# Kernel optimization log

Hardware: AMD Instinct MI355X
Metric: run time of the kernel (lower is better)

Reference implementation:

```python
import jax, jax.numpy as jnp
import numpy as np

DIM = 1024
HIDDEN = 4096
NUM_EXPERTS = 8
TOP_K = 2


def setup_inputs() -> dict:
    key = jax.random.key(0)
    ks = jax.random.split(key, 7)
    x = jax.random.normal(ks[0], (4, 2048, DIM), dtype=jnp.float32)
    # router Linear(dim, num_experts)
    Wr = jax.random.normal(ks[1], (DIM, NUM_EXPERTS), dtype=jnp.float32) / np.sqrt(DIM)
    br = jnp.zeros((NUM_EXPERTS,), dtype=jnp.float32)
    # stacked expert weights: Linear(dim, hidden) -> GELU -> Linear(hidden, dim)
    W1 = jax.random.normal(ks[2], (NUM_EXPERTS, DIM, HIDDEN), dtype=jnp.float32) / np.sqrt(DIM)
    b1 = jnp.zeros((NUM_EXPERTS, HIDDEN), dtype=jnp.float32)
    W2 = jax.random.normal(ks[3], (NUM_EXPERTS, HIDDEN, DIM), dtype=jnp.float32) / np.sqrt(HIDDEN)
    b2 = jnp.zeros((NUM_EXPERTS, DIM), dtype=jnp.float32)
    return {"x": x, "Wr": Wr, "br": br, "W1": W1, "b1": b1, "W2": W2, "b2": b2}


def reference(x, Wr, br, W1, b1, W2, b2):
    # router: g_x = W_e x ; p = softmax(g_x)
    logits = jnp.einsum('bsd,de->bse', x, Wr) + br            # [B,S,E]
    probs = jax.nn.softmax(logits, axis=-1)
    topk_probs, topk_idx = jax.lax.top_k(probs, TOP_K)        # [B,S,K]
    # dense compute-all-experts (faithful to torch.stack over experts)
    h = jnp.einsum('bsd,edh->bseh', x, W1) + b1               # [B,S,E,H]
    h = jax.nn.gelu(h, approximate=False)                      # torch nn.GELU default = exact erf
    expert_out = jnp.einsum('bseh,ehd->bsed', h, W2) + b2     # [B,S,E,D]
    # gather top-k expert outputs and mix
    selected = jnp.take_along_axis(expert_out, topk_idx[..., None], axis=2)  # [B,S,K,D]
    mixed = jnp.sum(topk_probs[..., None] * selected, axis=2)                # [B,S,D]
    return mixed, logits, probs, topk_idx, topk_probs
```

## Files before the change

### kernel.cpp

```cpp
#include <hip/hip_runtime.h>
#include <hip/hip_bf16.h>
#include <math.h>
#include <stdint.h>

#define DIMD 1024
#define HIDDEN 4096
#define NE 8
#define TOPK_ 2
#define T_TOKENS 8192
#define NROWS (T_TOKENS * TOPK_)
#define BM 128
#define BN 128
#define BK 64
#define MAXTILES (NROWS / BM + NE)
#define TGS 8
#define SPLITK 2

typedef __bf16 bf16_t;
typedef __bf16 bf16x8 __attribute__((ext_vector_type(8)));
typedef float f32x4 __attribute__((ext_vector_type(4)));

__device__ __forceinline__ void glds16(const void* g, void* l) {
    __builtin_amdgcn_global_load_lds(
        (const __attribute__((address_space(1))) unsigned int*)g,
        (__attribute__((address_space(3))) unsigned int*)l, 16, 0, 0);
}

__device__ __forceinline__ bf16x8 ldfrag(const char* lds_, int row, int kelem) {
    int byte = row * 128 + ((kelem * 2) ^ ((row & 7) << 4));
    return *reinterpret_cast<const bf16x8*>(lds_ + byte);
}

__device__ __forceinline__ int xcd_contig(int bid, int nwg) {
    int xcd = bid & 7;
    int lid = bid >> 3;
    int q = nwg >> 3, r = nwg & 7;
    int base = (xcd < r) ? xcd * (q + 1) : r * (q + 1) + (xcd - r) * q;
    return base + lid;
}

#define STAGE8(kb) do { \
    char* dA_ = lds + wid * 1024; \
    char* dB_ = lds + 16384 + wid * 1024; \
    glds16(ga0 + (kb), dA_);         glds16(gb0 + (kb), dB_); \
    glds16(ga1 + (kb), dA_ + 4096);  glds16(gb1 + (kb), dB_ + 4096); \
    glds16(ga2 + (kb), dA_ + 8192);  glds16(gb2 + (kb), dB_ + 8192); \
    glds16(ga3 + (kb), dA_ + 12288); glds16(gb3 + (kb), dB_ + 12288); \
} while (0)

#define COMPUTE64() do { \
    const char* Ab_ = lds; \
    const char* Bb_ = lds + 16384; \
    int rr_ = lane & 15, kk_ = (lane >> 4) * 8; \
    bf16x8 a_[4], b_[4]; \
    _Pragma("unroll") for (int m_ = 0; m_ < 4; ++m_) a_[m_] = ldfrag(Ab_, wr + m_ * 16 + rr_, kk_); \
    _Pragma("unroll") for (int n_ = 0; n_ < 4; ++n_) b_[n_] = ldfrag(Bb_, wc + n_ * 16 + rr_, kk_); \
    _Pragma("unroll") for (int m_ = 0; m_ < 4; ++m_) \
    _Pragma("unroll") for (int n_ = 0; n_ < 4; ++n_) \
        acc[m_][n_] = __builtin_amdgcn_mfma_f32_16x16x32_bf16(a_[m_], b_[n_], acc[m_][n_], 0, 0, 0); \
    _Pragma("unroll") for (int m_ = 0; m_ < 4; ++m_) a_[m_] = ldfrag(Ab_, wr + m_ * 16 + rr_, 32 + kk_); \
    _Pragma("unroll") for (int n_ = 0; n_ < 4; ++n_) b_[n_] = ldfrag(Bb_, wc + n_ * 16 + rr_, 32 + kk_); \
    _Pragma("unroll") for (int m_ = 0; m_ < 4; ++m_) \
    _Pragma("unroll") for (int n_ = 0; n_ < 4; ++n_) \
        acc[m_][n_] = __builtin_amdgcn_mfma_f32_16x16x32_bf16(a_[m_], b_[n_], acc[m_][n_], 0, 0, 0); \
} while (0)

#define GEMM_LOOP(nsteps) do { \
    for (int t_ = 0; t_ < (nsteps); ++t_) { \
        STAGE8(t_ * 128); \
        __syncthreads(); \
        COMPUTE64(); \
        __syncthreads(); \
    } \
} while (0)

__global__ __launch_bounds__(256) void router_kernel(
    const float* __restrict__ x, const float* __restrict__ Wr, const float* __restrict__ br,
    float* __restrict__ logits, float* __restrict__ probs,
    float* __restrict__ tidx, float* __restrict__ tprob,
    int* __restrict__ cnt, bf16_t* __restrict__ Xb)
{
    int wave = threadIdx.x >> 6;
    int lane = threadIdx.x & 63;
    int t = blockIdx.x * 4 + wave;
    if (t >= T_TOKENS) return;
    const float* xr = x + (size_t)t * DIMD;
    double acc[NE];
#pragma unroll
    for (int e = 0; e < NE; ++e) acc[e] = 0.0;
    for (int i = 0; i < DIMD / 64; ++i) {
        int d = i * 64 + lane;
        double xv = (double)xr[d];
        float4 w0 = *reinterpret_cast<const float4*>(Wr + d * NE);
        float4 w1 = *reinterpret_cast<const float4*>(Wr + d * NE + 4);
        acc[0] += xv * (double)w0.x; acc[1] += xv * (double)w0.y;
        acc[2] += xv * (double)w0.z; acc[3] += xv * (double)w0.w;
        acc[4] += xv * (double)w1.x; acc[5] += xv * (double)w1.y;
        acc[6] += xv * (double)w1.z; acc[7] += xv * (double)w1.w;
    }
#pragma unroll
    for (int s = 32; s >= 1; s >>= 1) {
#pragma unroll
        for (int e = 0; e < NE; ++e) acc[e] += __shfl_xor(acc[e], s, 64);
    }
    if (lane == 0) {
        double lg[NE], mx = -1e300;
#pragma unroll
        for (int e = 0; e < NE; ++e) { lg[e] = acc[e] + (double)br[e]; mx = fmax(mx, lg[e]); }
        int i0 = 0; double l0 = -1e300;
#pragma unroll
        for (int e = 0; e < NE; ++e) { if (lg[e] > l0) { l0 = lg[e]; i0 = e; } }
        int i1 = -1; double l1 = -1e300;
#pragma unroll
        for (int e = 0; e < NE; ++e) { if (e == i0) continue; if (lg[e] > l1) { l1 = lg[e]; i1 = e; } }
        float pe[NE], s = 0.f;
#pragma unroll
        for (int e = 0; e < NE; ++e) { pe[e] = __expf((float)(lg[e] - mx)); s += pe[e]; }
        float inv = 1.f / s;
#pragma unroll
        for (int e = 0; e < NE; ++e) {
            pe[e] *= inv;
            logits[t * NE + e] = (float)lg[e];
            probs[t * NE + e] = pe[e];
        }
        tidx[t * 2 + 0] = (float)i0; tidx[t * 2 + 1] = (float)i1;
        tprob[t * 2 + 0] = pe[i0];   tprob[t * 2 + 1] = pe[i1];
        atomicAdd(&cnt[i0], 1); atomicAdd(&cnt[i1], 1);
    }
#pragma unroll
    for (int j = 0; j < 2; ++j) {
        int i = (j * 64 + lane) * 8;
        float4 a = *reinterpret_cast<const float4*>(xr + i);
        float4 b = *reinterpret_cast<const float4*>(xr + i + 4);
        bf16x8 o;
        o[0] = (bf16_t)a.x; o[1] = (bf16_t)a.y; o[2] = (bf16_t)a.z; o[3] = (bf16_t)a.w;
        o[4] = (bf16_t)b.x; o[5] = (bf16_t)b.y; o[6] = (bf16_t)b.z; o[7] = (bf16_t)b.w;
        *reinterpret_cast<bf16x8*>(Xb + (size_t)t * DIMD + i) = o;
    }
}

__global__ __launch_bounds__(256) void transpose_kernel(
    const float* __restrict__ in, bf16_t* __restrict__ out, int K, int N)
{
    __shared__ float tile[64][33];
    int e = blockIdx.z;
    int k0 = blockIdx.x * 64;
    int n0 = blockIdx.y * 32;
    const float* ip = in + (size_t)e * K * N;
    bf16_t* op = out + (size_t)e * N * K;
    int t = threadIdx.x;
    int r = t >> 2;
    int c = (t & 3) * 8;
    float4 v0 = *reinterpret_cast<const float4*>(ip + (size_t)(k0 + r) * N + n0 + c);
    float4 v1 = *reinterpret_cast<const float4*>(ip + (size_t)(k0 + r) * N + n0 + c + 4);
    tile[r][c] = v0.x; tile[r][c + 1] = v0.y; tile[r][c + 2] = v0.z; tile[r][c + 3] = v0.w;
    tile[r][c + 4] = v1.x; tile[r][c + 5] = v1.y; tile[r][c + 6] = v1.z; tile[r][c + 7] = v1.w;
    __syncthreads();
    int nn = t >> 3;
    int kk = (t & 7) * 8;
    bf16x8 o;
#pragma unroll
    for (int j = 0; j < 8; ++j) o[j] = (bf16_t)tile[kk + j][nn];
    *reinterpret_cast<bf16x8*>(op + (size_t)(n0 + nn) * K + k0 + kk) = o;
}

__global__ __launch_bounds__(256) void prefix_kernel(
    const int* __restrict__ cnt, int* __restrict__ offsets,
    int* __restrict__ tileE, int* __restrict__ tileRow, int* __restrict__ numTiles)
{
    __shared__ int soff[NE + 1], scnt[NE];
    int t = threadIdx.x;
    if (t == 0) {
        int off = 0;
        for (int e = 0; e < NE; ++e) { scnt[e] = cnt[e]; soff[e] = off; off += scnt[e]; }
        soff[NE] = off;
        int nt = 0;
        for (int e = 0; e < NE; ++e) nt += (scnt[e] + BM - 1) / BM;
        *numTiles = nt;
    }
    __syncthreads();
    if (t <= NE) offsets[t] = soff[t];
    if (t < MAXTILES) {
        int acc = 0;
#pragma unroll
        for (int e = 0; e < NE; ++e) {
            int ntE = (scnt[e] + BM - 1) / BM;
            if (t < acc + ntE) { tileE[t] = e; tileRow[t] = soff[e] + (t - acc) * BM; return; }
            acc += ntE;
        }
    }
}

__global__ __launch_bounds__(256) void scatter_kernel(
    const float* __restrict__ tidx, const float* __restrict__ tprob,
    const int* __restrict__ offsets, int* __restrict__ gcursor,
    int* __restrict__ rowToken, float* __restrict__ rowProb)
{
    __shared__ int lcnt[NE], lbase[NE];
    int t = blockIdx.x * 256 + threadIdx.x;
    if (threadIdx.x < NE) lcnt[threadIdx.x] = 0;
    __syncthreads();
    int e0 = (int)tidx[t * 2 + 0], e1 = (int)tidx[t * 2 + 1];
    float p0 = tprob[t * 2 + 0],   p1 = tprob[t * 2 + 1];
    int r0l = atomicAdd(&lcnt[e0], 1);
    int r1l = atomicAdd(&lcnt[e1], 1);
    __syncthreads();
    if (threadIdx.x < NE) lbase[threadIdx.x] = atomicAdd(&gcursor[threadIdx.x], lcnt[threadIdx.x]);
    __syncthreads();
    int r0 = offsets[e0] + lbase[e0] + r0l;
    int r1 = offsets[e1] + lbase[e1] + r1l;
    rowToken[r0] = t; rowProb[r0] = p0;
    rowToken[r1] = t; rowProb[r1] = p1;
}

__global__ __launch_bounds__(256) void ffn1_kernel(
    const bf16_t* __restrict__ Xb, const bf16_t* __restrict__ W1T, const float* __restrict__ b1,
    const int* __restrict__ tileE, const int* __restrict__ tileRow, const int* __restrict__ numTiles,
    const int* __restrict__ offsets, const int* __restrict__ rowToken,
    bf16_t* __restrict__ h, int hc_base, int hc_len, int NB)
{
    int logical = xcd_contig(blockIdx.x, gridDim.x);
    int tg  = logical / (NB * TGS);
    int rem = logical % (NB * TGS);
    int nb  = rem / TGS;
    int ti  = rem % TGS;
    int tile = tg * TGS + ti;
    if (tile >= *numTiles) return;
    int e = tileE[tile];
    int row0 = tileRow[tile];
    int rend = offsets[e + 1];
    int n0 = nb * BN;
    int nglob = hc_base + n0;

    __shared__ __align__(16) char lds[32768];

    int tid = threadIdx.x;
    int lane = tid & 63;
    int wid = tid >> 6;
    int wr = (wid >> 1) * 64;
    int wc = (wid & 1) * 64;

    int srow = tid >> 3;
    int xc = (((tid & 7) ^ (srow & 7)) << 4);
    const char *ga0, *ga1, *ga2, *ga3, *gb0, *gb1, *gb2, *gb3;
    {
        int rl0 = srow, rl1 = 32 + srow, rl2 = 64 + srow, rl3 = 96 + srow;
        int g0 = row0 + rl0; if (g0 > NROWS - 1) g0 = NROWS - 1;
        int g1 = row0 + rl1; if (g1 > NROWS - 1) g1 = NROWS - 1;
        int g2 = row0 + rl2; if (g2 > NROWS - 1) g2 = NROWS - 1;
        int g3 = row0 + rl3; if (g3 > NROWS - 1) g3 = NROWS - 1;
        ga0 = (const char*)(Xb + (size_t)rowToken[g0] * DIMD) + xc;
        ga1 = (const char*)(Xb + (size_t)rowToken[g1] * DIMD) + xc;
        ga2 = (const char*)(Xb + (size_t)rowToken[g2] * DIMD) + xc;
        ga3 = (const char*)(Xb + (size_t)rowToken[g3] * DIMD) + xc;
        gb0 = (const char*)(W1T + ((size_t)e * HIDDEN + nglob + rl0) * DIMD) + xc;
        gb1 = (const char*)(W1T + ((size_t)e * HIDDEN + nglob + rl1) * DIMD) + xc;
        gb2 = (const char*)(W1T + ((size_t)e * HIDDEN + nglob + rl2) * DIMD) + xc;
        gb3 = (const char*)(W1T + ((size_t)e * HIDDEN + nglob + rl3) * DIMD) + xc;
    }

    f32x4 acc[4][4];
#pragma unroll
    for (int i = 0; i < 4; ++i)
#pragma unroll
        for (int j = 0; j < 4; ++j) acc[i][j] = f32x4{0.f, 0.f, 0.f, 0.f};

    GEMM_LOOP(DIMD / BK);

    int crow = (lane >> 4) * 4;
    int ccol = lane & 15;
#pragma unroll
    for (int m = 0; m < 4; ++m) {
#pragma unroll
        for (int n = 0; n < 4; ++n) {
            int col = wc + n * 16 + ccol;
            float bias = b1[e * HIDDEN + nglob + col];
#pragma unroll
            for (int r = 0; r < 4; ++r) {
                int row = row0 + wr + m * 16 + crow + r;
                if (row < rend) {
                    float v = acc[m][n][r] + bias;
                    float g = 0.5f * v * (1.0f + erff(v * 0.70710678118654752f));
                    h[(size_t)row * hc_len + n0 + col] = (bf16_t)g;
                }
            }
        }
    }
}

__global__ __launch_bounds__(256) void ffn2_kernel(
    const bf16_t* __restrict__ h, const bf16_t* __restrict__ W2T, const float* __restrict__ b2,
    const int* __restrict__ tileE, const int* __restrict__ tileRow, const int* __restrict__ numTiles,
    const int* __restrict__ offsets, const int* __restrict__ rowToken, const float* __restrict__ rowProb,
    float* __restrict__ mixed, int hc_base, int hc_len, int add_bias)
{
    const int NB = DIMD / BN;
    int logical = xcd_contig(blockIdx.x, gridDim.x);
    int z = logical / (MAXTILES * NB);
    int rem = logical % (MAXTILES * NB);
    int tile = rem / NB;
    int nb = rem % NB;
    if (tile >= *numTiles) return;
    int e = tileE[tile];
    int row0 = tileRow[tile];
    int rend = offsets[e + 1];
    int n0 = nb * BN;
    int khalf = hc_len / SPLITK;
    int khb = z * khalf * 2;

    __shared__ __align__(16) char lds[32768];

    int tid = threadIdx.x;
    int lane = tid & 63;
    int wid = tid >> 6;
    int wr = (wid >> 1) * 64;
    int wc = (wid & 1) * 64;

    int srow = tid >> 3;
    int xc = (((tid & 7) ^ (srow & 7)) << 4);
    const char *ga0, *ga1, *ga2, *ga3, *gb0, *gb1, *gb2, *gb3;
    {
        int rl0 = srow, rl1 = 32 + srow, rl2 = 64 + srow, rl3 = 96 + srow;
        int g0 = row0 + rl0; if (g0 > NROWS - 1) g0 = NROWS - 1;
        int g1 = row0 + rl1; if (g1 > NROWS - 1) g1 = NROWS - 1;
        int g2 = row0 + rl2; if (g2 > NROWS - 1) g2 = NROWS - 1;
        int g3 = row0 + rl3; if (g3 > NROWS - 1) g3 = NROWS - 1;
        ga0 = (const char*)(h + (size_t)g0 * hc_len) + khb + xc;
        ga1 = (const char*)(h + (size_t)g1 * hc_len) + khb + xc;
        ga2 = (const char*)(h + (size_t)g2 * hc_len) + khb + xc;
        ga3 = (const char*)(h + (size_t)g3 * hc_len) + khb + xc;
        gb0 = (const char*)(W2T + ((size_t)e * DIMD + n0 + rl0) * HIDDEN + hc_base) + khb + xc;
        gb1 = (const char*)(W2T + ((size_t)e * DIMD + n0 + rl1) * HIDDEN + hc_base) + khb + xc;
        gb2 = (const char*)(W2T + ((size_t)e * DIMD + n0 + rl2) * HIDDEN + hc_base) + khb + xc;
        gb3 = (const char*)(W2T + ((size_t)e * DIMD + n0 + rl3) * HIDDEN + hc_base) + khb + xc;
    }

    f32x4 acc[4][4];
#pragma unroll
    for (int i = 0; i < 4; ++i)
#pragma unroll
        for (int j = 0; j < 4; ++j) acc[i][j] = f32x4{0.f, 0.f, 0.f, 0.f};

    GEMM_LOOP(khalf / BK);

    int crow = (lane >> 4) * 4;
    int ccol = lane & 15;
    int dobias = add_bias && (z == 0);
#pragma unroll
    for (int m = 0; m < 4; ++m) {
#pragma unroll
        for (int n = 0; n < 4; ++n) {
            int col = wc + n * 16 + ccol;
            int dcol = n0 + col;
            float bias = dobias ? b2[e * DIMD + dcol] : 0.f;
#pragma unroll
            for (int r = 0; r < 4; ++r) {
                int row = row0 + wr + m * 16 + crow + r;
                if (row < rend) {
                    float v = acc[m][n][r] + bias;
                    float p = rowProb[row];
                    int tok = rowToken[row];
                    atomicAdd(&mixed[(size_t)tok * DIMD + dcol], p * v);
                }
            }
        }
    }
}

extern "C" void kernel_launch(void* const* d_in, const int* in_sizes, int n_in,
                              void* d_out, int out_size, void* d_ws, size_t ws_size,
                              hipStream_t stream)
{
    const float* x  = (const float*)d_in[0];
    const float* Wr = (const float*)d_in[1];
    const float* br = (const float*)d_in[2];
    const float* W1 = (const float*)d_in[3];
    const float* b1 = (const float*)d_in[4];
    const float* W2 = (const float*)d_in[5];
    const float* b2 = (const float*)d_in[6];

    float* out = (float*)d_out;
    float* mixed  = out;
    float* logits = out + (size_t)T_TOKENS * DIMD;
    float* probs  = logits + T_TOKENS * NE;
    float* tidx   = probs + T_TOKENS * NE;
    float* tprob  = tidx + T_TOKENS * TOPK_;

    char* p = (char*)d_ws;
    auto alloc = [&](size_t bytes) { char* r = p; p += (bytes + 255) & ~255ull; return r; };
    int*    small    = (int*)alloc(2 * NE * 4);
    int*    cnt      = small;
    int*    gcursor  = small + NE;
    int*    offsets  = (int*)alloc((NE + 1) * 4);
    int*    numTiles = (int*)alloc(4);
    int*    tileE    = (int*)alloc(MAXTILES * 4);
    int*    tileRow  = (int*)alloc(MAXTILES * 4);
    int*    rowToken = (int*)alloc(NROWS * 4);
    float*  rowProb  = (float*)alloc(NROWS * 4);
    bf16_t* W1T      = (bf16_t*)alloc((size_t)NE * HIDDEN * DIMD * 2);
    bf16_t* W2T      = (bf16_t*)alloc((size_t)NE * DIMD * HIDDEN * 2);
    bf16_t* Xb       = (bf16_t*)alloc((size_t)T_TOKENS * DIMD * 2);
    size_t used = (size_t)(p - (char*)d_ws);
    size_t remain = ws_size > used ? ws_size - used : 0;
    int hc = HIDDEN;
    while (hc > 512 && (size_t)NROWS * hc * 2 > remain) hc >>= 1;
    bf16_t* hbuf = (bf16_t*)alloc((size_t)NROWS * hc * 2);

    hipMemsetAsync(small, 0, 2 * NE * 4, stream);
    hipMemsetAsync(mixed, 0, (size_t)T_TOKENS * DIMD * 4, stream);

    router_kernel<<<T_TOKENS / 4, 256, 0, stream>>>(x, Wr, br, logits, probs, tidx, tprob, cnt, Xb);
    transpose_kernel<<<dim3(DIMD / 64, HIDDEN / 32, NE), 256, 0, stream>>>(W1, W1T, DIMD, HIDDEN);
    transpose_kernel<<<dim3(HIDDEN / 64, DIMD / 32, NE), 256, 0, stream>>>(W2, W2T, HIDDEN, DIMD);
    prefix_kernel<<<1, 256, 0, stream>>>(cnt, offsets, tileE, tileRow, numTiles);
    scatter_kernel<<<T_TOKENS / 256, 256, 0, stream>>>(tidx, tprob, offsets, gcursor, rowToken, rowProb);

    for (int c0 = 0; c0 < HIDDEN; c0 += hc) {
        int nb1 = hc / BN;
        ffn1_kernel<<<MAXTILES * nb1, 256, 0, stream>>>(
            Xb, W1T, b1, tileE, tileRow, numTiles, offsets, rowToken, hbuf, c0, hc, nb1);
        ffn2_kernel<<<MAXTILES * (DIMD / BN) * SPLITK, 256, 0, stream>>>(
            hbuf, W2T, b2, tileE, tileRow, numTiles, offsets, rowToken, rowProb,
            mixed, c0, hc, c0 == 0 ? 1 : 0);
    }
}
```

Before: 831.8 us.

## Use 256x256 tiles with 8-wave double-buffered phased MFMA pipeline

Both expert GEMMs move from 128x128 tiles with 4 waves and single-buffered LDS to 256x256 tiles with 8 waves. The new loop double-buffers LDS (128 KB) and splits each K step into four sub-phases, issuing global-to-LDS loads for the next buffer between them. Explicit vmcnt waits, s_barrier and setprio control the schedule. The aim is to raise arithmetic intensity and hide global load latency behind MFMA work, at the cost of more padding waste per expert tile, fewer blocks, and heavy register and LDS pressure.

Result: slower. 1.002 ms (+20.4%).

```diff
diff --git a/kernel.cpp b/kernel.cpp
--- a/kernel.cpp
+++ b/kernel.cpp
@@ -9,11 +9,11 @@
 #define TOPK_ 2
 #define T_TOKENS 8192
 #define NROWS (T_TOKENS * TOPK_)
-#define BM 128
-#define BN 128
+#define BM 256
+#define BN 256
 #define BK 64
-#define MAXTILES (NROWS / BM + NE)
-#define TGS 8
+#define MAXT (NROWS / BM + NE)
+#define TGS 4
 #define SPLITK 2
 
 typedef __bf16 bf16_t;
@@ -39,38 +39,67 @@
     return base + lid;
 }
 
-#define STAGE8(kb) do { \
-    char* dA_ = lds + wid * 1024; \
-    char* dB_ = lds + 16384 + wid * 1024; \
-    glds16(ga0 + (kb), dA_);         glds16(gb0 + (kb), dB_); \
-    glds16(ga1 + (kb), dA_ + 4096);  glds16(gb1 + (kb), dB_ + 4096); \
-    glds16(ga2 + (kb), dA_ + 8192);  glds16(gb2 + (kb), dB_ + 8192); \
-    glds16(ga3 + (kb), dA_ + 12288); glds16(gb3 + (kb), dB_ + 12288); \
+#define SA(B, KB, I) glds16(pa##I + (KB), lds + (B) * 65536 + (I) * 8192 + wid * 1024)
+#define SB(B, KB, I) glds16(pb##I + (KB), lds + (B) * 65536 + 32768 + (I) * 8192 + wid * 1024)
+
+#define VM0 do { \
+    __builtin_amdgcn_sched_barrier(0); \
+    asm volatile("s_waitcnt vmcnt(0)" ::: "memory"); \
+    __builtin_amdgcn_sched_barrier(0); \
 } while (0)
 
-#define COMPUTE64() do { \
-    const char* Ab_ = lds; \
-    const char* Bb_ = lds + 16384; \
-    int rr_ = lane & 15, kk_ = (lane >> 4) * 8; \
-    bf16x8 a_[4], b_[4]; \
-    _Pragma("unroll") for (int m_ = 0; m_ < 4; ++m_) a_[m_] = ldfrag(Ab_, wr + m_ * 16 + rr_, kk_); \
-    _Pragma("unroll") for (int n_ = 0; n_ < 4; ++n_) b_[n_] = ldfrag(Bb_, wc + n_ * 16 + rr_, kk_); \
+#define PH(B, MQ, NQ, PRE, POST) do { \
+    const char* Ab_ = lds + (B) * 65536; \
+    const char* Bb_ = lds + (B) * 65536 + 32768; \
+    bf16x8 av_[4][2], bv_[2][2]; \
     _Pragma("unroll") for (int m_ = 0; m_ < 4; ++m_) \
-    _Pragma("unroll") for (int n_ = 0; n_ < 4; ++n_) \
-        acc[m_][n_] = __builtin_amdgcn_mfma_f32_16x16x32_bf16(a_[m_], b_[n_], acc[m_][n_], 0, 0, 0); \
-    _Pragma("unroll") for (int m_ = 0; m_ < 4; ++m_) a_[m_] = ldfrag(Ab_, wr + m_ * 16 + rr_, 32 + kk_); \
-    _Pragma("unroll") for (int n_ = 0; n_ < 4; ++n_) b_[n_] = ldfrag(Bb_, wc + n_ * 16 + rr_, 32 + kk_); \
+    _Pragma("unroll") for (int ks_ = 0; ks_ < 2; ++ks_) \
+        av_[m_][ks_] = ldfrag(Ab_, wr + (MQ) * 64 + m_ * 16 + rr, ks_ * 32 + k4); \
+    _Pragma("unroll") for (int n_ = 0; n_ < 2; ++n_) \
+    _Pragma("unroll") for (int ks_ = 0; ks_ < 2; ++ks_) \
+        bv_[n_][ks_] = ldfrag(Bb_, wc + (NQ) * 32 + n_ * 16 + rr, ks_ * 32 + k4); \
+    PRE; \
+    __builtin_amdgcn_s_setprio(1); \
+    _Pragma("unroll") for (int ks_ = 0; ks_ < 2; ++ks_) \
     _Pragma("unroll") for (int m_ = 0; m_ < 4; ++m_) \
-    _Pragma("unroll") for (int n_ = 0; n_ < 4; ++n_) \
-        acc[m_][n_] = __builtin_amdgcn_mfma_f32_16x16x32_bf16(a_[m_], b_[n_], acc[m_][n_], 0, 0, 0); \
+    _Pragma("unroll") for (int n_ = 0; n_ < 2; ++n_) \
+        acc[(MQ) * 4 + m_][(NQ) * 2 + n_] = __builtin_amdgcn_mfma_f32_16x16x32_bf16( \
+            av_[m_][ks_], bv_[n_][ks_], acc[(MQ) * 4 + m_][(NQ) * 2 + n_], 0, 0, 0); \
+    __builtin_amdgcn_s_setprio(0); \
+    POST; \
+    __builtin_amdgcn_sched_barrier(0); \
+    __builtin_amdgcn_s_barrier(); \
+    __builtin_amdgcn_sched_barrier(0); \
 } while (0)
 
-#define GEMM_LOOP(nsteps) do { \
-    for (int t_ = 0; t_ < (nsteps); ++t_) { \
-        STAGE8(t_ * 128); \
-        __syncthreads(); \
-        COMPUTE64(); \
-        __syncthreads(); \
+#define GEMM8PH(nt) do { \
+    SA(0, 0, 0); SA(0, 0, 1); SA(0, 0, 2); SA(0, 0, 3); \
+    SB(0, 0, 0); SB(0, 0, 1); SB(0, 0, 2); SB(0, 0, 3); \
+    SA(1, 128, 0); SA(1, 128, 1); SA(1, 128, 2); SA(1, 128, 3); \
+    SB(1, 128, 0); SB(1, 128, 1); SB(1, 128, 2); SB(1, 128, 3); \
+    __builtin_amdgcn_sched_barrier(0); \
+    asm volatile("s_waitcnt vmcnt(8)" ::: "memory"); \
+    __builtin_amdgcn_sched_barrier(0); \
+    __builtin_amdgcn_s_barrier(); \
+    __builtin_amdgcn_sched_barrier(0); \
+     \
+    PH(0, 0, 0, , ); PH(0, 0, 1, , ); PH(0, 1, 0, , ); PH(0, 1, 1, , VM0); \
+    PH(1, 0, 0, SA(0, 256, 0); SA(0, 256, 1); SA(0, 256, 2), ); \
+    PH(1, 0, 1, SA(0, 256, 3); SB(0, 256, 0); SB(0, 256, 1), ); \
+    PH(1, 1, 0, SB(0, 256, 2); SB(0, 256, 3), ); \
+    PH(1, 1, 1, , VM0); \
+    for (int i_ = 1; i_ < (nt) / 2; ++i_) { \
+        int kbO = (2 * i_ + 1) * 128; \
+        int ke_ = 2 * i_ + 2; if (ke_ > (nt) - 1) ke_ = (nt) - 1; \
+        int kbE = ke_ * 128; \
+        PH(0, 0, 0, SA(1, kbO, 0); SA(1, kbO, 1); SA(1, kbO, 2), ); \
+        PH(0, 0, 1, SA(1, kbO, 3); SB(1, kbO, 0); SB(1, kbO, 1), ); \
+        PH(0, 1, 0, SB(1, kbO, 2); SB(1, kbO, 3), ); \
+        PH(0, 1, 1, , VM0); \
+        PH(1, 0, 0, SA(0, kbE, 0); SA(0, kbE, 1); SA(0, kbE, 2), ); \
+        PH(1, 0, 1, SA(0, kbE, 3); SB(0, kbE, 0); SB(0, kbE, 1), ); \
+        PH(1, 1, 0, SB(0, kbE, 2); SB(0, kbE, 3), ); \
+        PH(1, 1, 1, , VM0); \
     } \
 } while (0)
 
@@ -180,7 +209,7 @@
     }
     __syncthreads();
     if (t <= NE) offsets[t] = soff[t];
-    if (t < MAXTILES) {
+    if (t < MAXT) {
         int acc = 0;
 #pragma unroll
         for (int e = 0; e < NE; ++e) {
@@ -213,7 +242,7 @@
     rowToken[r1] = t; rowProb[r1] = p1;
 }
 
-__global__ __launch_bounds__(256) void ffn1_kernel(
+__global__ __launch_bounds__(512, 2) void ffn1_kernel(
     const bf16_t* __restrict__ Xb, const bf16_t* __restrict__ W1T, const float* __restrict__ b1,
     const int* __restrict__ tileE, const int* __restrict__ tileRow, const int* __restrict__ numTiles,
     const int* __restrict__ offsets, const int* __restrict__ rowToken,
@@ -232,45 +261,46 @@
     int n0 = nb * BN;
     int nglob = hc_base + n0;
 
-    __shared__ __align__(16) char lds[32768];
+    __shared__ __align__(16) char lds[131072];
 
     int tid = threadIdx.x;
     int lane = tid & 63;
     int wid = tid >> 6;
-    int wr = (wid >> 1) * 64;
-    int wc = (wid & 1) * 64;
+    int wr = (wid >> 2) * 128;
+    int wc = (wid & 3) * 64;
+    int rr = lane & 15;
+    int k4 = (lane >> 4) * 8;
 
     int srow = tid >> 3;
     int xc = (((tid & 7) ^ (srow & 7)) << 4);
-    const char *ga0, *ga1, *ga2, *ga3, *gb0, *gb1, *gb2, *gb3;
+    const char *pa0, *pa1, *pa2, *pa3, *pb0, *pb1, *pb2, *pb3;
     {
-        int rl0 = srow, rl1 = 32 + srow, rl2 = 64 + srow, rl3 = 96 + srow;
-        int g0 = row0 + rl0; if (g0 > NROWS - 1) g0 = NROWS - 1;
-        int g1 = row0 + rl1; if (g1 > NROWS - 1) g1 = NROWS - 1;
-        int g2 = row0 + rl2; if (g2 > NROWS - 1) g2 = NROWS - 1;
-        int g3 = row0 + rl3; if (g3 > NROWS - 1) g3 = NROWS - 1;
-        ga0 = (const char*)(Xb + (size_t)rowToken[g0] * DIMD) + xc;
-        ga1 = (const char*)(Xb + (size_t)rowToken[g1] * DIMD) + xc;
-        ga2 = (const char*)(Xb + (size_t)rowToken[g2] * DIMD) + xc;
-        ga3 = (const char*)(Xb + (size_t)rowToken[g3] * DIMD) + xc;
-        gb0 = (const char*)(W1T + ((size_t)e * HIDDEN + nglob + rl0) * DIMD) + xc;
-        gb1 = (const char*)(W1T + ((size_t)e * HIDDEN + nglob + rl1) * DIMD) + xc;
-        gb2 = (const char*)(W1T + ((size_t)e * HIDDEN + nglob + rl2) * DIMD) + xc;
-        gb3 = (const char*)(W1T + ((size_t)e * HIDDEN + nglob + rl3) * DIMD) + xc;
-    }
-
-    f32x4 acc[4][4];
-#pragma unroll
-    for (int i = 0; i < 4; ++i)
+        int g0 = row0 + srow;       if (g0 > NROWS - 1) g0 = NROWS - 1;
+        int g1 = row0 + 64 + srow;  if (g1 > NROWS - 1) g1 = NROWS - 1;
+        int g2 = row0 + 128 + srow; if (g2 > NROWS - 1) g2 = NROWS - 1;
+        int g3 = row0 + 192 + srow; if (g3 > NROWS - 1) g3 = NROWS - 1;
+        pa0 = (const char*)(Xb + (size_t)rowToken[g0] * DIMD) + xc;
+        pa1 = (const char*)(Xb + (size_t)rowToken[g1] * DIMD) + xc;
+        pa2 = (const char*)(Xb + (size_t)rowToken[g2] * DIMD) + xc;
+        pa3 = (const char*)(Xb + (size_t)rowToken[g3] * DIMD) + xc;
+        pb0 = (const char*)(W1T + ((size_t)e * HIDDEN + nglob + srow) * DIMD) + xc;
+        pb1 = (const char*)(W1T + ((size_t)e * HIDDEN + nglob + 64 + srow) * DIMD) + xc;
+        pb2 = (const char*)(W1T + ((size_t)e * HIDDEN + nglob + 128 + srow) * DIMD) + xc;
+        pb3 = (const char*)(W1T + ((size_t)e * HIDDEN + nglob + 192 + srow) * DIMD) + xc;
+    }
+
+    f32x4 acc[8][4];
+#pragma unroll
+    for (int i = 0; i < 8; ++i)
 #pragma unroll
         for (int j = 0; j < 4; ++j) acc[i][j] = f32x4{0.f, 0.f, 0.f, 0.f};
 
-    GEMM_LOOP(DIMD / BK);
+    GEMM8PH(DIMD / BK);
 
     int crow = (lane >> 4) * 4;
     int ccol = lane & 15;
 #pragma unroll
-    for (int m = 0; m < 4; ++m) {
+    for (int m = 0; m < 8; ++m) {
 #pragma unroll
         for (int n = 0; n < 4; ++n) {
             int col = wc + n * 16 + ccol;
@@ -288,7 +318,7 @@
     }
 }
 
-__global__ __launch_bounds__(256) void ffn2_kernel(
+__global__ __launch_bounds__(512, 2) void ffn2_kernel(
     const bf16_t* __restrict__ h, const bf16_t* __restrict__ W2T, const float* __restrict__ b2,
     const int* __restrict__ tileE, const int* __restrict__ tileRow, const int* __restrict__ numTiles,
     const int* __restrict__ offsets, const int* __restrict__ rowToken, const float* __restrict__ rowProb,
@@ -296,8 +326,8 @@
 {
     const int NB = DIMD / BN;
     int logical = xcd_contig(blockIdx.x, gridDim.x);
-    int z = logical / (MAXTILES * NB);
-    int rem = logical % (MAXTILES * NB);
+    int z = logical / (MAXT * NB);
+    int rem = logical % (MAXT * NB);
     int tile = rem / NB;
     int nb = rem % NB;
     if (tile >= *numTiles) return;
@@ -308,46 +338,47 @@
     int khalf = hc_len / SPLITK;
     int khb = z * khalf * 2;
 
-    __shared__ __align__(16) char lds[32768];
+    __shared__ __align__(16) char lds[131072];
 
     int tid = threadIdx.x;
     int lane = tid & 63;
     int wid = tid >> 6;
-    int wr = (wid >> 1) * 64;
-    int wc = (wid & 1) * 64;
+    int wr = (wid >> 2) * 128;
+    int wc = (wid & 3) * 64;
+    int rr = lane & 15;
+    int k4 = (lane >> 4) * 8;
 
     int srow = tid >> 3;
     int xc = (((tid & 7) ^ (srow & 7)) << 4);
-    const char *ga0, *ga1, *ga2, *ga3, *gb0, *gb1, *gb2, *gb3;
+    const char *pa0, *pa1, *pa2, *pa3, *pb0, *pb1, *pb2, *pb3;
     {
-        int rl0 = srow, rl1 = 32 + srow, rl2 = 64 + srow, rl3 = 96 + srow;
-        int g0 = row0 + rl0; if (g0 > NROWS - 1) g0 = NROWS - 1;
-        int g1 = row0 + rl1; if (g1 > NROWS - 1) g1 = NROWS - 1;
-        int g2 = row0 + rl2; if (g2 > NROWS - 1) g2 = NROWS - 1;
-        int g3 = row0 + rl3; if (g3 > NROWS - 1) g3 = NROWS - 1;
-        ga0 = (const char*)(h + (size_t)g0 * hc_len) + khb + xc;
-        ga1 = (const char*)(h + (size_t)g1 * hc_len) + khb + xc;
-        ga2 = (const char*)(h + (size_t)g2 * hc_len) + khb + xc;
-        ga3 = (const char*)(h + (size_t)g3 * hc_len) + khb + xc;
-        gb0 = (const char*)(W2T + ((size_t)e * DIMD + n0 + rl0) * HIDDEN + hc_base) + khb + xc;
-        gb1 = (const char*)(W2T + ((size_t)e * DIMD + n0 + rl1) * HIDDEN + hc_base) + khb + xc;
-        gb2 = (const char*)(W2T + ((size_t)e * DIMD + n0 + rl2) * HIDDEN + hc_base) + khb + xc;
-        gb3 = (const char*)(W2T + ((size_t)e * DIMD + n0 + rl3) * HIDDEN + hc_base) + khb + xc;
-    }
-
-    f32x4 acc[4][4];
-#pragma unroll
-    for (int i = 0; i < 4; ++i)
+        int g0 = row0 + srow;       if (g0 > NROWS - 1) g0 = NROWS - 1;
+        int g1 = row0 + 64 + srow;  if (g1 > NROWS - 1) g1 = NROWS - 1;
+        int g2 = row0 + 128 + srow; if (g2 > NROWS - 1) g2 = NROWS - 1;
+        int g3 = row0 + 192 + srow; if (g3 > NROWS - 1) g3 = NROWS - 1;
+        pa0 = (const char*)(h + (size_t)g0 * hc_len) + khb + xc;
+        pa1 = (const char*)(h + (size_t)g1 * hc_len) + khb + xc;
+        pa2 = (const char*)(h + (size_t)g2 * hc_len) + khb + xc;
+        pa3 = (const char*)(h + (size_t)g3 * hc_len) + khb + xc;
+        pb0 = (const char*)(W2T + ((size_t)e * DIMD + n0 + srow) * HIDDEN + hc_base) + khb + xc;
+        pb1 = (const char*)(W2T + ((size_t)e * DIMD + n0 + 64 + srow) * HIDDEN + hc_base) + khb + xc;
+        pb2 = (const char*)(W2T + ((size_t)e * DIMD + n0 + 128 + srow) * HIDDEN + hc_base) + khb + xc;
+        pb3 = (const char*)(W2T + ((size_t)e * DIMD + n0 + 192 + srow) * HIDDEN + hc_base) + khb + xc;
+    }
+
+    f32x4 acc[8][4];
+#pragma unroll
+    for (int i = 0; i < 8; ++i)
 #pragma unroll
         for (int j = 0; j < 4; ++j) acc[i][j] = f32x4{0.f, 0.f, 0.f, 0.f};
 
-    GEMM_LOOP(khalf / BK);
+    GEMM8PH(khalf / BK);
 
     int crow = (lane >> 4) * 4;
     int ccol = lane & 15;
     int dobias = add_bias && (z == 0);
 #pragma unroll
-    for (int m = 0; m < 4; ++m) {
+    for (int m = 0; m < 8; ++m) {
 #pragma unroll
         for (int n = 0; n < 4; ++n) {
             int col = wc + n * 16 + ccol;
@@ -393,8 +424,8 @@
     int*    gcursor  = small + NE;
     int*    offsets  = (int*)alloc((NE + 1) * 4);
     int*    numTiles = (int*)alloc(4);
-    int*    tileE    = (int*)alloc(MAXTILES * 4);
-    int*    tileRow  = (int*)alloc(MAXTILES * 4);
+    int*    tileE    = (int*)alloc(MAXT * 4);
+    int*    tileRow  = (int*)alloc(MAXT * 4);
     int*    rowToken = (int*)alloc(NROWS * 4);
     float*  rowProb  = (float*)alloc(NROWS * 4);
     bf16_t* W1T      = (bf16_t*)alloc((size_t)NE * HIDDEN * DIMD * 2);
@@ -417,9 +448,9 @@
 
     for (int c0 = 0; c0 < HIDDEN; c0 += hc) {
         int nb1 = hc / BN;
-        ffn1_kernel<<<MAXTILES * nb1, 256, 0, stream>>>(
+        ffn1_kernel<<<MAXT * nb1, 512, 0, stream>>>(
             Xb, W1T, b1, tileE, tileRow, numTiles, offsets, rowToken, hbuf, c0, hc, nb1);
-        ffn2_kernel<<<MAXTILES * (DIMD / BN) * SPLITK, 256, 0, stream>>>(
+        ffn2_kernel<<<MAXT * (DIMD / BN) * SPLITK, 512, 0, stream>>>(
             hbuf, W2T, b2, tileE, tileRow, numTiles, offsets, rowToken, rowProb,
             mixed, c0, hc, c0 == 0 ? 1 : 0);
     }
```

## Widen GEMM tiles to 128x256 with 8 waves per block

Applied to the files above, without the earlier changes.

Doubles the N tile width of both expert GEMMs from 128 to 256. Blocks grow to 512 threads (8 waves, each still computing a 64x64 sub-tile) and LDS grows to 48KB, with the staging and compute macros rewritten to match. Each loaded A tile is now reused across twice as many output columns, cutting A-side global traffic and the number of blocks. The cost is fewer, larger blocks, which can lower occupancy and balance, especially in ffn2 where the grid is already small.

After: 828.5 us. No clear change (-0.4%).

```diff
diff --git a/kernel.cpp b/kernel.cpp
--- a/kernel.cpp
+++ b/kernel.cpp
@@ -10,7 +10,7 @@
 #define T_TOKENS 8192
 #define NROWS (T_TOKENS * TOPK_)
 #define BM 128
-#define BN 128
+#define BN 256
 #define BK 64
 #define MAXTILES (NROWS / BM + NE)
 #define TGS 8
@@ -39,37 +39,34 @@
     return base + lid;
 }
 
-#define STAGE8(kb) do { \
-    char* dA_ = lds + wid * 1024; \
-    char* dB_ = lds + 16384 + wid * 1024; \
-    glds16(ga0 + (kb), dA_);         glds16(gb0 + (kb), dB_); \
-    glds16(ga1 + (kb), dA_ + 4096);  glds16(gb1 + (kb), dB_ + 4096); \
-    glds16(ga2 + (kb), dA_ + 8192);  glds16(gb2 + (kb), dB_ + 8192); \
-    glds16(ga3 + (kb), dA_ + 12288); glds16(gb3 + (kb), dB_ + 12288); \
+#define STAGE6(kb) do { \
+    glds16(pa0 + (kb), lds + wid * 1024); \
+    glds16(pa1 + (kb), lds + 8192 + wid * 1024); \
+    glds16(pb0 + (kb), lds + 16384 + wid * 1024); \
+    glds16(pb1 + (kb), lds + 16384 + 8192 + wid * 1024); \
+    glds16(pb2 + (kb), lds + 16384 + 16384 + wid * 1024); \
+    glds16(pb3 + (kb), lds + 16384 + 24576 + wid * 1024); \
 } while (0)
 
-#define COMPUTE64() do { \
-    const char* Ab_ = lds; \
-    const char* Bb_ = lds + 16384; \
-    int rr_ = lane & 15, kk_ = (lane >> 4) * 8; \
-    bf16x8 a_[4], b_[4]; \
-    _Pragma("unroll") for (int m_ = 0; m_ < 4; ++m_) a_[m_] = ldfrag(Ab_, wr + m_ * 16 + rr_, kk_); \
-    _Pragma("unroll") for (int n_ = 0; n_ < 4; ++n_) b_[n_] = ldfrag(Bb_, wc + n_ * 16 + rr_, kk_); \
-    _Pragma("unroll") for (int m_ = 0; m_ < 4; ++m_) \
-    _Pragma("unroll") for (int n_ = 0; n_ < 4; ++n_) \
-        acc[m_][n_] = __builtin_amdgcn_mfma_f32_16x16x32_bf16(a_[m_], b_[n_], acc[m_][n_], 0, 0, 0); \
-    _Pragma("unroll") for (int m_ = 0; m_ < 4; ++m_) a_[m_] = ldfrag(Ab_, wr + m_ * 16 + rr_, 32 + kk_); \
-    _Pragma("unroll") for (int n_ = 0; n_ < 4; ++n_) b_[n_] = ldfrag(Bb_, wc + n_ * 16 + rr_, 32 + kk_); \
-    _Pragma("unroll") for (int m_ = 0; m_ < 4; ++m_) \
-    _Pragma("unroll") for (int n_ = 0; n_ < 4; ++n_) \
-        acc[m_][n_] = __builtin_amdgcn_mfma_f32_16x16x32_bf16(a_[m_], b_[n_], acc[m_][n_], 0, 0, 0); \
+#define COMPUTE() do { \
+    _Pragma("unroll") for (int ks_ = 0; ks_ < 2; ++ks_) { \
+        int kk_ = ks_ * 32 + k4; \
+        bf16x8 b_[4], a_[4]; \
+        _Pragma("unroll") for (int n_ = 0; n_ < 4; ++n_) \
+            b_[n_] = ldfrag(lds + 16384, wc + n_ * 16 + rr, kk_); \
+        _Pragma("unroll") for (int m_ = 0; m_ < 4; ++m_) \
+            a_[m_] = ldfrag(lds, wr + m_ * 16 + rr, kk_); \
+        _Pragma("unroll") for (int m_ = 0; m_ < 4; ++m_) \
+        _Pragma("unroll") for (int n_ = 0; n_ < 4; ++n_) \
+            acc[m_][n_] = __builtin_amdgcn_mfma_f32_16x16x32_bf16(a_[m_], b_[n_], acc[m_][n_], 0, 0, 0); \
+    } \
 } while (0)
 
 #define GEMM_LOOP(nsteps) do { \
     for (int t_ = 0; t_ < (nsteps); ++t_) { \
-        STAGE8(t_ * 128); \
+        STAGE6(t_ * 128); \
         __syncthreads(); \
-        COMPUTE64(); \
+        COMPUTE(); \
         __syncthreads(); \
     } \
 } while (0)
@@ -213,7 +210,7 @@
     rowToken[r1] = t; rowProb[r1] = p1;
 }
 
-__global__ __launch_bounds__(256) void ffn1_kernel(
+__global__ __launch_bounds__(512) void ffn1_kernel(
     const bf16_t* __restrict__ Xb, const bf16_t* __restrict__ W1T, const float* __restrict__ b1,
     const int* __restrict__ tileE, const int* __restrict__ tileRow, const int* __restrict__ numTiles,
     const int* __restrict__ offsets, const int* __restrict__ rowToken,
@@ -232,31 +229,28 @@
     int n0 = nb * BN;
     int nglob = hc_base + n0;
 
-    __shared__ __align__(16) char lds[32768];
+    __shared__ __align__(16) char lds[49152];
 
     int tid = threadIdx.x;
     int lane = tid & 63;
     int wid = tid >> 6;
-    int wr = (wid >> 1) * 64;
-    int wc = (wid & 1) * 64;
+    int wr = (wid >> 2) * 64;
+    int wc = (wid & 3) * 64;
+    int rr = lane & 15;
+    int k4 = (lane >> 4) * 8;
 
     int srow = tid >> 3;
     int xc = (((tid & 7) ^ (srow & 7)) << 4);
-    const char *ga0, *ga1, *ga2, *ga3, *gb0, *gb1, *gb2, *gb3;
+    const char *pa0, *pa1, *pb0, *pb1, *pb2, *pb3;
     {
-        int rl0 = srow, rl1 = 32 + srow, rl2 = 64 + srow, rl3 = 96 + srow;
-        int g0 = row0 + rl0; if (g0 > NROWS - 1) g0 = NROWS - 1;
-        int g1 = row0 + rl1; if (g1 > NROWS - 1) g1 = NROWS - 1;
-        int g2 = row0 + rl2; if (g2 > NROWS - 1) g2 = NROWS - 1;
-        int g3 = row0 + rl3; if (g3 > NROWS - 1) g3 = NROWS - 1;
-        ga0 = (const char*)(Xb + (size_t)rowToken[g0] * DIMD) + xc;
-        ga1 = (const char*)(Xb + (size_t)rowToken[g1] * DIMD) + xc;
-        ga2 = (const char*)(Xb + (size_t)rowToken[g2] * DIMD) + xc;
-        ga3 = (const char*)(Xb + (size_t)rowToken[g3] * DIMD) + xc;
-        gb0 = (const char*)(W1T + ((size_t)e * HIDDEN + nglob + rl0) * DIMD) + xc;
-        gb1 = (const char*)(W1T + ((size_t)e * HIDDEN + nglob + rl1) * DIMD) + xc;
-        gb2 = (const char*)(W1T + ((size_t)e * HIDDEN + nglob + rl2) * DIMD) + xc;
-        gb3 = (const char*)(W1T + ((size_t)e * HIDDEN + nglob + rl3) * DIMD) + xc;
+        int g0 = row0 + srow;      if (g0 > NROWS - 1) g0 = NROWS - 1;
+        int g1 = row0 + 64 + srow; if (g1 > NROWS - 1) g1 = NROWS - 1;
+        pa0 = (const char*)(Xb + (size_t)rowToken[g0] * DIMD) + xc;
+        pa1 = (const char*)(Xb + (size_t)rowToken[g1] * DIMD) + xc;
+        pb0 = (const char*)(W1T + ((size_t)e * HIDDEN + nglob + srow) * DIMD) + xc;
+        pb1 = (const char*)(W1T + ((size_t)e * HIDDEN + nglob + 64 + srow) * DIMD) + xc;
+        pb2 = (const char*)(W1T + ((size_t)e * HIDDEN + nglob + 128 + srow) * DIMD) + xc;
+        pb3 = (const char*)(W1T + ((size_t)e * HIDDEN + nglob + 192 + srow) * DIMD) + xc;
     }
 
     f32x4 acc[4][4];
@@ -288,7 +282,7 @@
     }
 }
 
-__global__ __launch_bounds__(256) void ffn2_kernel(
+__global__ __launch_bounds__(512) void ffn2_kernel(
     const bf16_t* __restrict__ h, const bf16_t* __restrict__ W2T, const float* __restrict__ b2,
     const int* __restrict__ tileE, const int* __restrict__ tileRow, const int* __restrict__ numTiles,
     const int* __restrict__ offsets, const int* __restrict__ rowToken, const float* __restrict__ rowProb,
@@ -308,31 +302,28 @@
     int khalf = hc_len / SPLITK;
     int khb = z * khalf * 2;
 
-    __shared__ __align__(16) char lds[32768];
+    __shared__ __align__(16) char lds[49152];
 
     int tid = threadIdx.x;
     int lane = tid & 63;
     int wid = tid >> 6;
-    int wr = (wid >> 1) * 64;
-    int wc = (wid & 1) * 64;
+    int wr = (wid >> 2) * 64;
+    int wc = (wid & 3) * 64;
+    int rr = lane & 15;
+    int k4 = (lane >> 4) * 8;
 
     int srow = tid >> 3;
     int xc = (((tid & 7) ^ (srow & 7)) << 4);
-    const char *ga0, *ga1, *ga2, *ga3, *gb0, *gb1, *gb2, *gb3;
+    const char *pa0, *pa1, *pb0, *pb1, *pb2, *pb3;
     {
-        int rl0 = srow, rl1 = 32 + srow, rl2 = 64 + srow, rl3 = 96 + srow;
-        int g0 = row0 + rl0; if (g0 > NROWS - 1) g0 = NROWS - 1;
-        int g1 = row0 + rl1; if (g1 > NROWS - 1) g1 = NROWS - 1;
-        int g2 = row0 + rl2; if (g2 > NROWS - 1) g2 = NROWS - 1;
-        int g3 = row0 + rl3; if (g3 > NROWS - 1) g3 = NROWS - 1;
-        ga0 = (const char*)(h + (size_t)g0 * hc_len) + khb + xc;
-        ga1 = (const char*)(h + (size_t)g1 * hc_len) + khb + xc;
-        ga2 = (const char*)(h + (size_t)g2 * hc_len) + khb + xc;
-        ga3 = (const char*)(h + (size_t)g3 * hc_len) + khb + xc;
-        gb0 = (const char*)(W2T + ((size_t)e * DIMD + n0 + rl0) * HIDDEN + hc_base) + khb + xc;
-        gb1 = (const char*)(W2T + ((size_t)e * DIMD + n0 + rl1) * HIDDEN + hc_base) + khb + xc;
-        gb2 = (const char*)(W2T + ((size_t)e * DIMD + n0 + rl2) * HIDDEN + hc_base) + khb + xc;
-        gb3 = (const char*)(W2T + ((size_t)e * DIMD + n0 + rl3) * HIDDEN + hc_base) + khb + xc;
+        int g0 = row0 + srow;      if (g0 > NROWS - 1) g0 = NROWS - 1;
+        int g1 = row0 + 64 + srow; if (g1 > NROWS - 1) g1 = NROWS - 1;
+        pa0 = (const char*)(h + (size_t)g0 * hc_len) + khb + xc;
+        pa1 = (const char*)(h + (size_t)g1 * hc_len) + khb + xc;
+        pb0 = (const char*)(W2T + ((size_t)e * DIMD + n0 + srow) * HIDDEN + hc_base) + khb + xc;
+        pb1 = (const char*)(W2T + ((size_t)e * DIMD + n0 + 64 + srow) * HIDDEN + hc_base) + khb + xc;
+        pb2 = (const char*)(W2T + ((size_t)e * DIMD + n0 + 128 + srow) * HIDDEN + hc_base) + khb + xc;
+        pb3 = (const char*)(W2T + ((size_t)e * DIMD + n0 + 192 + srow) * HIDDEN + hc_base) + khb + xc;
     }
 
     f32x4 acc[4][4];
@@ -417,9 +408,9 @@
 
     for (int c0 = 0; c0 < HIDDEN; c0 += hc) {
         int nb1 = hc / BN;
-        ffn1_kernel<<<MAXTILES * nb1, 256, 0, stream>>>(
+        ffn1_kernel<<<MAXTILES * nb1, 512, 0, stream>>>(
             Xb, W1T, b1, tileE, tileRow, numTiles, offsets, rowToken, hbuf, c0, hc, nb1);
-        ffn2_kernel<<<MAXTILES * (DIMD / BN) * SPLITK, 256, 0, stream>>>(
+        ffn2_kernel<<<MAXTILES * (DIMD / BN) * SPLITK, 512, 0, stream>>>(
             hbuf, W2T, b2, tileE, tileRow, numTiles, offsets, rowToken, rowProb,
             mixed, c0, hc, c0 == 0 ? 1 : 0);
     }
```
